# Performance work log

Hardware: AMD Instinct MI355X
Metric: run time of the kernel (lower is better)

## Reference

```python
import jax, jax.numpy as jnp
import numpy as np

V, E, H, ENC2, L_LAYERS = 1024, 512, 1024, 1024, 3
SOS, EOS = 1, 2


def lstm_cell(x, h, c, W_ih, W_hh, b_ih, b_hh):
    # PyTorch LSTMCell: gates ordered i, f, g, o
    gates = x @ W_ih.T + b_ih + h @ W_hh.T + b_hh
    i, f, g, o = jnp.split(gates, 4, axis=-1)
    i = jax.nn.sigmoid(i)
    f = jax.nn.sigmoid(f)
    g = jnp.tanh(g)
    o = jax.nn.sigmoid(o)
    c = f * c + i * g
    h = o * jnp.tanh(c)
    return h, c


def setup_inputs() -> dict:
    key = jax.random.key(0)
    ks = jax.random.split(key, 20)
    s = 0.05
    inp = {
        'tokens': jax.random.randint(ks[0], (16, 256), 0, V),
        'encoder_outputs': jax.random.normal(ks[1], (16, 512, ENC2), jnp.float32),
        'embedding': jax.random.normal(ks[2], (V, E), jnp.float32) * s,
        # layer 0: input = embedding + encoder context
        'W_ih0': jax.random.normal(ks[3], (4 * H, E + ENC2), jnp.float32) * s,
        'W_hh0': jax.random.normal(ks[4], (4 * H, H), jnp.float32) * s,
        'b_ih0': jnp.zeros((4 * H,), jnp.float32),
        'b_hh0': jnp.zeros((4 * H,), jnp.float32),
        'W_ih1': jax.random.normal(ks[5], (4 * H, H), jnp.float32) * s,
        'W_hh1': jax.random.normal(ks[6], (4 * H, H), jnp.float32) * s,
        'b_ih1': jnp.zeros((4 * H,), jnp.float32),
        'b_hh1': jnp.zeros((4 * H,), jnp.float32),
        'W_ih2': jax.random.normal(ks[7], (4 * H, H), jnp.float32) * s,
        'W_hh2': jax.random.normal(ks[8], (4 * H, H), jnp.float32) * s,
        'b_ih2': jnp.zeros((4 * H,), jnp.float32),
        'b_hh2': jnp.zeros((4 * H,), jnp.float32),
        'W1': jax.random.normal(ks[9], (H, ENC2 + H), jnp.float32) * s,
        'b1': jnp.zeros((H,), jnp.float32),
        'W2': jax.random.normal(ks[10], (V, H), jnp.float32) * s,
        'b2': jnp.zeros((V,), jnp.float32),
    }
    return inp


def reference(tokens, encoder_outputs, embedding,
              W_ih0, W_hh0, b_ih0, b_hh0,
              W_ih1, W_hh1, b_ih1, b_hh1,
              W_ih2, W_hh2, b_ih2, b_hh2,
              W1, b1, W2, b2):
    B, L = tokens.shape
    dtype = encoder_outputs.dtype
    # teacher forcing sequences: dec_in = [sos, y], dec_out = [y, eos]
    dec_in = jnp.concatenate([jnp.full((B, 1), SOS, tokens.dtype), tokens], axis=1)   # [B, T]
    dec_out = jnp.concatenate([tokens, jnp.full((B, 1), EOS, tokens.dtype)], axis=1)  # [B, T]
    T = L + 1

    emb = embedding[dec_in]  # [B, T, E]
    # NOTE: the original forward feeds initial_context (zeros) as the LSTM input
    # context at EVERY step (it is never updated), so the recurrence does not
    # depend on attention and can be scanned independently.
    xs = jnp.concatenate([emb, jnp.zeros((B, T, ENC2), dtype)], axis=-1)  # [B, T, E+ENC2]
    xs = jnp.swapaxes(xs, 0, 1)  # time-major [T, B, E+ENC2]

    z = jnp.zeros((B, H), dtype)
    init = (z, z, z, z, z, z)

    def step(carry, x_t):
        h0, c0, h1, c1, h2, c2 = carry
        h0, c0 = lstm_cell(x_t, h0, c0, W_ih0, W_hh0, b_ih0, b_hh0)
        h1, c1 = lstm_cell(h0, h1, c1, W_ih1, W_hh1, b_ih1, b_hh1)
        h2, c2 = lstm_cell(h1, h2, c2, W_ih2, W_hh2, b_ih2, b_hh2)
        return (h0, c0, h1, c1, h2, c2), h2

    _, hs = jax.lax.scan(step, init, xs)      # [T, B, H]
    hs = jnp.swapaxes(hs, 0, 1)               # [B, T, H]

    # dot-product attention over encoder outputs (vectorized over all steps)
    scores = jnp.einsum('bth,bsh->bts', hs, encoder_outputs)   # [B, T, S]
    attn = jax.nn.softmax(scores, axis=-1)
    ctx = jnp.einsum('bts,bsh->bth', attn, encoder_outputs)    # [B, T, ENC2]

    mlp_in = jnp.concatenate([hs, ctx], axis=-1)               # [B, T, H+ENC2]
    hidden = jnp.tanh(mlp_in @ W1.T + b1)
    logits = hidden @ W2.T + b2                                # [B, T, V]

    logp = jax.nn.log_softmax(logits, axis=-1)
    nll = -jnp.take_along_axis(logp, dec_out[..., None], axis=-1)[..., 0]
    return jnp.mean(nll)
```

## Files before the change

### kernel.cpp

```cpp
#include <hip/hip_runtime.h>
#include <math.h>


namespace {
constexpr int TT = 257;
constexpr int BT = 4112;
constexpr int NSTEP = 259;
constexpr int NWG = 256;

constexpr size_t OFF_EMBB = 0;
constexpr size_t OFF_H0H  = 524288;
constexpr size_t OFF_H1H  = 4751360;
constexpr size_t OFF_H2H  = 8978432;
constexpr size_t OFF_ENCB = 0;
constexpr size_t OFF_ENCT = 13205504;
constexpr size_t OFF_W1B  = 21594112;
constexpr size_t OFF_W2B  = 23691264;
constexpr size_t OFF_SC   = 24739840;
constexpr size_t OFF_CTX  = 26845184;
constexpr size_t OFF_HID  = 31055872;
constexpr size_t OFF_LG   = OFF_SC;
constexpr size_t END_BF   = 35266560;
constexpr size_t OFF_INT_BYTES = END_BF * 2;
constexpr int    ARRIVE_I0     = 12352;
constexpr int    GO_I0         = ARRIVE_I0 + 256 * 32;
constexpr size_t TOTAL_BYTES   = OFF_INT_BYTES + (GO_I0 + 16) * 4;
constexpr unsigned SPIN_CAP    = 1u << 22;
}

typedef __attribute__((ext_vector_type(8))) short bf16x8;
typedef __attribute__((ext_vector_type(4))) float f32x4;

__device__ __forceinline__ float bf2f(ushort u) {
    union { unsigned int v; float f; } x; x.v = ((unsigned int)u) << 16; return x.f;
}
__device__ __forceinline__ ushort f2bf(float f) {
    union { float f; unsigned int v; } x; x.f = f;
    return (ushort)((x.v + 0x7fff + ((x.v >> 16) & 1)) >> 16);
}
__device__ __forceinline__ float sigm(float x) { return 1.f / (1.f + __expf(-x)); }

__global__ void k_fail(float* out) { out[0] = -123456.0f; }

__global__ __launch_bounds__(256) void k_init(const int* __restrict__ tokens,
                                              const float* __restrict__ emb,
                                              ushort* __restrict__ wsb,
                                              float* __restrict__ out)
{
    int i = blockIdx.x * 256 + threadIdx.x;
    int* dec_in  = (int*)((char*)wsb + OFF_INT_BYTES);
    int* dec_out = dec_in + 4112;
    int* hsrow   = dec_in + 8224;
    unsigned* flags = (unsigned*)(dec_in + ARRIVE_I0);
    {
        size_t e = (size_t)i * 8;
        float4 a = *(const float4*)(emb + e);
        float4 b = *(const float4*)(emb + e + 4);
        uint4 o;
        o.x = (unsigned)f2bf(a.x) | ((unsigned)f2bf(a.y) << 16);
        o.y = (unsigned)f2bf(a.z) | ((unsigned)f2bf(a.w) << 16);
        o.z = (unsigned)f2bf(b.x) | ((unsigned)f2bf(b.y) << 16);
        o.w = (unsigned)f2bf(b.z) | ((unsigned)f2bf(b.w) << 16);
        *(uint4*)(wsb + OFF_EMBB + e) = o;
    }
    if (i < 16384) {
        wsb[OFF_H0H + i] = 0; wsb[OFF_H1H + i] = 0; wsb[OFF_H2H + i] = 0;
    }
    if (i < 4112) {
        int t = i >> 4, b = i & 15;
        dec_in[i] = (t == 0) ? 1 : tokens[b * 256 + (t - 1)];
        int bb = i / 257, tt = i % 257;
        dec_out[i] = (tt < 256) ? tokens[bb * 256 + tt] : 2;
        hsrow[i] = (tt + 1) * 16 + bb;
    }
    if (i < 256 * 32 + 16) flags[i] = 0u;
    if (i == 0) out[0] = 0.f;
}

__global__ __launch_bounds__(1024, 4) void k_rec_persist(
    ushort* __restrict__ wsb,
    const float* __restrict__ Whh0, const float* __restrict__ Wih0,
    const float* __restrict__ Wih1, const float* __restrict__ Whh1,
    const float* __restrict__ Wih2, const float* __restrict__ Whh2,
    const float* __restrict__ bih0, const float* __restrict__ bhh0,
    const float* __restrict__ bih1, const float* __restrict__ bhh1,
    const float* __restrict__ bih2, const float* __restrict__ bhh2,
    const int* __restrict__ dec_in,
    unsigned* __restrict__ arrive, unsigned* __restrict__ go)
{
    __shared__ float p[16][16][17];

    int tid = threadIdx.x;
    int u = blockIdx.x;
    int w = tid >> 6, lane = tid & 63, l15 = lane & 15, quad = lane >> 4;

    int cell, g0, gcnt;
    if (w < 4)       { cell = 0; g0 = w * 12; gcnt = 12; }
    else if (w < 10) { int wi = w - 4;  cell = 1;
                       g0 = (wi < 4) ? wi * 11 : 44 + (wi - 4) * 10;
                       gcnt = (wi < 4) ? 11 : 10; }
    else             { int wi = w - 10; cell = 2;
                       g0 = (wi < 4) ? wi * 11 : 44 + (wi - 4) * 10;
                       gcnt = (wi < 4) ? 11 : 10; }

    int gt = l15 >> 2, s4 = l15 & 3;
    size_t wrow = (size_t)(gt * 1024 + u * 4 + s4);

    bf16x8 wreg[12];
    #pragma unroll
    for (int gi = 0; gi < 12; ++gi) {
        if (gi < gcnt) {
            int g = g0 + gi;
            const float* src;
            if (cell == 0)
                src = (g < 32) ? Whh0 + wrow * 1024 + (size_t)g * 32
                               : Wih0 + wrow * 1536 + (size_t)(g - 32) * 32;
            else if (cell == 1)
                src = (g < 32) ? Wih1 + wrow * 1024 + (size_t)g * 32
                               : Whh1 + wrow * 1024 + (size_t)(g - 32) * 32;
            else
                src = (g < 32) ? Wih2 + wrow * 1024 + (size_t)g * 32
                               : Whh2 + wrow * 1024 + (size_t)(g - 32) * 32;
            src += quad * 8;
            float4 a = *(const float4*)src;
            float4 b = *(const float4*)(src + 4);
            bf16x8 v;
            v[0] = (short)f2bf(a.x); v[1] = (short)f2bf(a.y);
            v[2] = (short)f2bf(a.z); v[3] = (short)f2bf(a.w);
            v[4] = (short)f2bf(b.x); v[5] = (short)f2bf(b.y);
            v[6] = (short)f2bf(b.z); v[7] = (short)f2bf(b.w);
            wreg[gi] = v;
        }
    }

    int cellE = tid >> 6;
    int sub = tid & 63, bE = sub & 15, sE = sub >> 4;
    int colE = u * 4 + sE;
    float bsum[4] = {0.f, 0.f, 0.f, 0.f};
    float cst = 0.f;
    ushort* hE = nullptr;
    int wloE = 0, whiE = 0;
    if (tid < 192) {
        const float* biE = (cellE == 0) ? bih0 : (cellE == 1) ? bih1 : bih2;
        const float* bhE = (cellE == 0) ? bhh0 : (cellE == 1) ? bhh1 : bhh2;
        #pragma unroll
        for (int gq = 0; gq < 4; ++gq)
            bsum[gq] = biE[gq * 1024 + colE] + bhE[gq * 1024 + colE];
        hE = wsb + ((cellE == 0) ? OFF_H0H : (cellE == 1) ? OFF_H1H : OFF_H2H);
        wloE = (cellE == 0) ? 0 : (cellE == 1) ? 4 : 10;
        whiE = (cellE == 0) ? 4 : (cellE == 1) ? 10 : 16;
    }

    ushort* h0h = wsb + OFF_H0H;
    ushort* h1h = wsb + OFF_H1H;
    ushort* h2h = wsb + OFF_H2H;
    const ushort* embB = wsb + OFF_EMBB;
    size_t aoff = (size_t)l15 * 1024 + quad * 8;

    int tokv = 0;
    if (cell == 0) tokv = dec_in[l15];

    for (int d = 0; d < NSTEP; ++d) {
        int t = d - cell;
        f32x4 acc = {0.f, 0.f, 0.f, 0.f};
        if (t >= 0 && t < TT) {
            const ushort* a0p;
            const ushort* a1p;
            if (cell == 0) {
                a0p = h0h + (size_t)t * 16384 + aoff;
                a1p = embB + (size_t)tokv * 512 + quad * 8;
                int tn = (t + 1 < TT) ? (t + 1) : (TT - 1);
                tokv = dec_in[tn * 16 + l15];
            } else if (cell == 1) {
                a0p = h0h + (size_t)(t + 1) * 16384 + aoff;
                a1p = h1h + (size_t)t * 16384 + aoff;
            } else {
                a0p = h1h + (size_t)(t + 1) * 16384 + aoff;
                a1p = h2h + (size_t)t * 16384 + aoff;
            }
            #pragma unroll
            for (int gi = 0; gi < 12; ++gi) {
                if (gi < gcnt) {
                    int g = g0 + gi;
                    bf16x8 af = (g < 32)
                        ? *(const bf16x8*)(a0p + (size_t)g * 32)
                        : *(const bf16x8*)(a1p + (size_t)(g - 32) * 32);
                    acc = __builtin_amdgcn_mfma_f32_16x16x32_bf16(
                        af, wreg[gi], acc, 0, 0, 0);
                }
            }
        }
        #pragma unroll
        for (int r = 0; r < 4; ++r) p[w][quad * 4 + r][l15] = acc[r];
        __syncthreads();

        if (tid < 192) {
            int tE = d - cellE;
            if (tE >= 0 && tE < TT) {
                float gv[4];
                #pragma unroll
                for (int gq = 0; gq < 4; ++gq) {
                    float a2 = bsum[gq];
                    for (int ww = wloE; ww < whiE; ++ww)
                        a2 += p[ww][bE][gq * 4 + sE];
                    gv[gq] = a2;
                }
                float ig = sigm(gv[0]), fg = sigm(gv[1]);
                float gg = tanhf(gv[2]), og = sigm(gv[3]);
                cst = fg * cst + ig * gg;
                ushort hus = f2bf(og * tanhf(cst));
                unsigned hi = __shfl_down((unsigned)hus, 16, 64);
                if ((sE & 1) == 0) {
                    unsigned* hp = (unsigned*)(hE + (size_t)(tE + 1) * 16384
                                               + (size_t)bE * 1024 + colE);
                    __hip_atomic_store(hp, (unsigned)hus | (hi << 16),
                                       __ATOMIC_RELAXED, __HIP_MEMORY_SCOPE_AGENT);
                }
            }
        }

        asm volatile("s_waitcnt vmcnt(0)" ::: "memory");
        __syncthreads();
        unsigned stamp = (unsigned)(d + 1);
        if (u == 0) {
            if (tid > 0 && tid < 256) {
                unsigned spins = 0;
                while (__hip_atomic_load(arrive + tid * 32, __ATOMIC_RELAXED,
                                         __HIP_MEMORY_SCOPE_AGENT) < stamp) {
                    if (++spins > SPIN_CAP) break;
                }
            }
            __syncthreads();
            if (tid == 0)
                __hip_atomic_store(go, stamp, __ATOMIC_RELAXED,
                                   __HIP_MEMORY_SCOPE_AGENT);
        } else {
            if (tid == 0) {
                __hip_atomic_store(arrive + u * 32, stamp, __ATOMIC_RELAXED,
                                   __HIP_MEMORY_SCOPE_AGENT);
                unsigned spins = 0;
                while (__hip_atomic_load(go, __ATOMIC_RELAXED,
                                         __HIP_MEMORY_SCOPE_AGENT) < stamp) {
                    __builtin_amdgcn_s_sleep(1);
                    if (++spins > SPIN_CAP) break;
                }
            }
            __syncthreads();
        }
    }
}

__global__ __launch_bounds__(256) void k_cvt_flat(const float* __restrict__ src,
                                                  ushort* __restrict__ dst)
{
    size_t e = ((size_t)blockIdx.x * 256 + threadIdx.x) * 8;
    float4 a = *(const float4*)(src + e);
    float4 b = *(const float4*)(src + e + 4);
    uint4 o;
    o.x = (unsigned)f2bf(a.x) | ((unsigned)f2bf(a.y) << 16);
    o.y = (unsigned)f2bf(a.z) | ((unsigned)f2bf(a.w) << 16);
    o.z = (unsigned)f2bf(b.x) | ((unsigned)f2bf(b.y) << 16);
    o.w = (unsigned)f2bf(b.z) | ((unsigned)f2bf(b.w) << 16);
    *(uint4*)(dst + e) = o;
}

__global__ __launch_bounds__(256) void k_enc_t(const float* __restrict__ enc,
                                               ushort* __restrict__ encT)
{
    __shared__ float tile[32][33];
    int b = blockIdx.z, s0 = blockIdx.x * 32, h0 = blockIdx.y * 32;
    int tx = threadIdx.x & 31, ty = threadIdx.x >> 5;
    const float* src = enc + (size_t)b * 524288;
    #pragma unroll
    for (int i = 0; i < 4; i++) {
        int s = s0 + ty + i * 8;
        tile[ty + i * 8][tx] = src[(size_t)s * 1024 + h0 + tx];
    }
    __syncthreads();
    ushort* dst = encT + (size_t)b * 524288;
    #pragma unroll
    for (int i = 0; i < 4; i++) {
        int h = h0 + ty + i * 8;
        dst[(size_t)h * 512 + s0 + tx] = f2bf(tile[tx][ty + i * 8]);
    }
}

__global__ __launch_bounds__(256) void k_gemm_bb(
    const ushort* __restrict__ A, int lda, long sA, const int* __restrict__ aIdx,
    const ushort* __restrict__ B, int ldb, long sB,
    ushort* __restrict__ C, int ldc, long sC,
    int M, int K, int accum)
{
    int z = blockIdx.z;
    const ushort* Ab = A + (size_t)z * sA;
    const ushort* Bb = B + (size_t)z * sB;
    ushort* Cb = C + (size_t)z * sC;
    int m0 = blockIdx.y * 64, n0 = blockIdx.x * 64;
    int tid = threadIdx.x, w = tid >> 6, lane = tid & 63;
    int l15 = lane & 15, quad = lane >> 4;
    int am = m0 + w * 16 + l15;
    int ar = (am < M) ? (aIdx ? aIdx[am] : am) : (aIdx ? aIdx[0] : 0);
    const ushort* ap = Ab + (size_t)ar * lda + quad * 8;
    const ushort* bp = Bb + (size_t)(n0 + l15) * ldb + quad * 8;
    f32x4 acc[4] = {{0.f,0.f,0.f,0.f},{0.f,0.f,0.f,0.f},{0.f,0.f,0.f,0.f},{0.f,0.f,0.f,0.f}};
    for (int k0 = 0; k0 < K; k0 += 32) {
        bf16x8 af = *(const bf16x8*)(ap + k0);
        #pragma unroll
        for (int j = 0; j < 4; j++) {
            bf16x8 bfb = *(const bf16x8*)(bp + (size_t)j * 16 * ldb + k0);
            acc[j] = __builtin_amdgcn_mfma_f32_16x16x32_bf16(af, bfb, acc[j], 0, 0, 0);
        }
    }
    #pragma unroll
    for (int j = 0; j < 4; j++)
        #pragma unroll
        for (int r = 0; r < 4; r++) {
            int row = m0 + w * 16 + quad * 4 + r;
            if (row < M) {
                ushort* cp = Cb + (size_t)row * ldc + n0 + j * 16 + l15;
                float v = acc[j][r];
                if (accum) v += bf2f(*cp);
                *cp = f2bf(v);
            }
        }
}

__global__ __launch_bounds__(256) void k_softmax_b(ushort* __restrict__ sc)
{
    __shared__ float red[4];
    ushort* p = sc + (size_t)blockIdx.x * 512;
    int tid = threadIdx.x;
    float a = bf2f(p[tid]), b = bf2f(p[tid + 256]);
    float m = fmaxf(a, b);
    for (int o = 32; o; o >>= 1) m = fmaxf(m, __shfl_xor(m, o, 64));
    if ((tid & 63) == 0) red[tid >> 6] = m;
    __syncthreads();
    m = fmaxf(fmaxf(red[0], red[1]), fmaxf(red[2], red[3]));
    __syncthreads();
    float ea = __expf(a - m), eb = __expf(b - m);
    float s = ea + eb;
    for (int o = 32; o; o >>= 1) s += __shfl_xor(s, o, 64);
    if ((tid & 63) == 0) red[tid >> 6] = s;
    __syncthreads();
    s = red[0] + red[1] + red[2] + red[3];
    float inv = 1.f / s;
    p[tid] = f2bf(ea * inv);
    p[tid + 256] = f2bf(eb * inv);
}

__global__ __launch_bounds__(256) void k_tanh_bias_b(ushort* __restrict__ hid,
                                                     const float* __restrict__ b1)
{
    size_t i = (size_t)blockIdx.x * 256 + threadIdx.x;
    hid[i] = f2bf(tanhf(bf2f(hid[i]) + b1[i & 1023]));
}

__global__ __launch_bounds__(256) void k_loss_b(const ushort* __restrict__ logits,
                                                const float* __restrict__ b2,
                                                const int* __restrict__ dec_out_m,
                                                float* __restrict__ out)
{
    __shared__ float red[4];
    int m = blockIdx.x;
    const ushort* p = logits + (size_t)m * 1024;
    int tid = threadIdx.x;
    float v0 = bf2f(p[tid]) + b2[tid];
    float v1 = bf2f(p[tid + 256]) + b2[tid + 256];
    float v2 = bf2f(p[tid + 512]) + b2[tid + 512];
    float v3 = bf2f(p[tid + 768]) + b2[tid + 768];
    float mx = fmaxf(fmaxf(v0, v1), fmaxf(v2, v3));
    for (int o = 32; o; o >>= 1) mx = fmaxf(mx, __shfl_xor(mx, o, 64));
    if ((tid & 63) == 0) red[tid >> 6] = mx;
    __syncthreads();
    mx = fmaxf(fmaxf(red[0], red[1]), fmaxf(red[2], red[3]));
    __syncthreads();
    float s = __expf(v0 - mx) + __expf(v1 - mx) + __expf(v2 - mx) + __expf(v3 - mx);
    for (int o = 32; o; o >>= 1) s += __shfl_xor(s, o, 64);
    if ((tid & 63) == 0) red[tid >> 6] = s;
    __syncthreads();
    if (tid == 0) {
        float ssum = red[0] + red[1] + red[2] + red[3];
        int tgt = dec_out_m[m];
        float tv = bf2f(p[tgt]) + b2[tgt];
        atomicAdd(out, (mx + logf(ssum) - tv) * (1.0f / 4112.0f));
    }
}

extern "C" void kernel_launch(void* const* d_in, const int* in_sizes, int n_in,
                              void* d_out, int out_size, void* d_ws, size_t ws_size,
                              hipStream_t stream)
{
    const int*   tokens = (const int*)d_in[0];
    const float* enc    = (const float*)d_in[1];
    const float* emb    = (const float*)d_in[2];
    const float* Wih0   = (const float*)d_in[3];
    const float* Whh0   = (const float*)d_in[4];
    const float* bih0   = (const float*)d_in[5];
    const float* bhh0   = (const float*)d_in[6];
    const float* Wih1   = (const float*)d_in[7];
    const float* Whh1   = (const float*)d_in[8];
    const float* bih1   = (const float*)d_in[9];
    const float* bhh1   = (const float*)d_in[10];
    const float* Wih2   = (const float*)d_in[11];
    const float* Whh2   = (const float*)d_in[12];
    const float* bih2   = (const float*)d_in[13];
    const float* bhh2   = (const float*)d_in[14];
    const float* W1     = (const float*)d_in[15];
    const float* b1     = (const float*)d_in[16];
    const float* W2     = (const float*)d_in[17];
    const float* b2     = (const float*)d_in[18];

    float* out = (float*)d_out;
    if (ws_size < TOTAL_BYTES) { k_fail<<<1, 1, 0, stream>>>(out); return; }

    ushort* wsb  = (ushort*)d_ws;
    ushort* h2h  = wsb + OFF_H2H;
    ushort* sc   = wsb + OFF_SC;
    ushort* ctx  = wsb + OFF_CTX;
    ushort* hid  = wsb + OFF_HID;
    ushort* lg   = wsb + OFF_LG;
    ushort* encB = wsb + OFF_ENCB;
    ushort* encT = wsb + OFF_ENCT;
    ushort* W1b  = wsb + OFF_W1B;
    ushort* W2b  = wsb + OFF_W2B;
    int* dec_in  = (int*)((char*)d_ws + OFF_INT_BYTES);
    int* dec_out = dec_in + 4112;
    int* hsrow   = dec_in + 8224;
    unsigned* arrive = (unsigned*)(dec_in + ARRIVE_I0);
    unsigned* go     = (unsigned*)(dec_in + GO_I0);

    k_init<<<256, 256, 0, stream>>>(tokens, emb, wsb, out);

    k_rec_persist<<<NWG, 1024, 0, stream>>>(wsb, Whh0, Wih0, Wih1, Whh1,
                                            Wih2, Whh2, bih0, bhh0, bih1, bhh1,
                                            bih2, bhh2, dec_in, arrive, go);

    k_cvt_flat<<<4096, 256, 0, stream>>>(enc, encB);
    k_enc_t<<<dim3(16, 32, 16), 256, 0, stream>>>(enc, encT);
    k_cvt_flat<<<1024, 256, 0, stream>>>(W1, W1b);
    k_cvt_flat<<<512, 256, 0, stream>>>(W2, W2b);

    k_gemm_bb<<<dim3(8, 5, 16), 256, 0, stream>>>(h2h + 16384, 16384, 1024, nullptr,
                                                  encB, 1024, 524288,
                                                  sc, 512, 131584, TT, 1024, 0);
    k_softmax_b<<<4112, 256, 0, stream>>>(sc);
    k_gemm_bb<<<dim3(16, 5, 16), 256, 0, stream>>>(sc, 512, 131584, nullptr,
                                                   encT, 512, 524288,
                                                   ctx, 1024, 263168, TT, 512, 0);
    k_gemm_bb<<<dim3(16, 65, 1), 256, 0, stream>>>(h2h, 1024, 0, hsrow,
                                                   W1b, 2048, 0,
                                                   hid, 1024, 0, BT, 1024, 0);
    k_gemm_bb<<<dim3(16, 65, 1), 256, 0, stream>>>(ctx, 1024, 0, nullptr,
                                                   W1b + 1024, 2048, 0,
                                                   hid, 1024, 0, BT, 1024, 1);
    k_tanh_bias_b<<<16448, 256, 0, stream>>>(hid, b1);
    k_gemm_bb<<<dim3(16, 65, 1), 256, 0, stream>>>(hid, 1024, 0, nullptr,
                                                   W2b, 1024, 0,
                                                   lg, 1024, 0, BT, 1024, 0);
    k_loss_b<<<4112, 256, 0, stream>>>(lg, b2, dec_out, out);
}
```

Before: 3.083 ms.

## Fuse W1 two-part GEMM with bias and tanh; widen recurrent h stores

Replaces the two accumulating W1 GEMMs and the separate tanh+bias pass with one dual-input GEMM kernel that applies bias and tanh in its epilogue. This removes a bf16 round trip of the hidden buffer and two kernel launches. Separately, the recurrent kernel now packs four bf16 hidden values into one 64-bit atomic store instead of two per 32-bit store, halving the store count. The dual kernel has no LDS tiling, so global load efficiency is the same as the old GEMM.

Result: no change. 3.132 ms (+1.6%).

```diff
diff --git a/kernel.cpp b/kernel.cpp
--- a/kernel.cpp
+++ b/kernel.cpp
@@ -209,12 +209,16 @@
                 float gg = tanhf(gv[2]), og = sigm(gv[3]);
                 cst = fg * cst + ig * gg;
                 ushort hus = f2bf(og * tanhf(cst));
-                unsigned hi = __shfl_down((unsigned)hus, 16, 64);
-                if ((sE & 1) == 0) {
-                    unsigned* hp = (unsigned*)(hE + (size_t)(tE + 1) * 16384
-                                               + (size_t)bE * 1024 + colE);
-                    __hip_atomic_store(hp, (unsigned)hus | (hi << 16),
-                                       __ATOMIC_RELAXED, __HIP_MEMORY_SCOPE_AGENT);
+                unsigned pair  = (unsigned)hus
+                               | (__shfl_down((unsigned)hus, 16, 64) << 16);
+                unsigned pair2 = __shfl_down(pair, 32, 64);
+                if (sE == 0) {
+                    unsigned long long v = (unsigned long long)pair
+                                         | ((unsigned long long)pair2 << 32);
+                    unsigned long long* hp = (unsigned long long*)
+                        (hE + (size_t)(tE + 1) * 16384 + (size_t)bE * 1024 + colE);
+                    __hip_atomic_store(hp, v, __ATOMIC_RELAXED,
+                                       __HIP_MEMORY_SCOPE_AGENT);
                 }
             }
         }
@@ -325,6 +329,49 @@
         }
 }
 
+__global__ __launch_bounds__(256) void k_gemm_dual(
+    const ushort* __restrict__ A1, const int* __restrict__ aIdx,
+    const ushort* __restrict__ A2,
+    const ushort* __restrict__ B1, const ushort* __restrict__ B2,
+    const float* __restrict__ bias, ushort* __restrict__ C, int M)
+{
+    int m0 = blockIdx.y * 64, n0 = blockIdx.x * 64;
+    int tid = threadIdx.x, w = tid >> 6, lane = tid & 63;
+    int l15 = lane & 15, quad = lane >> 4;
+    int am = m0 + w * 16 + l15;
+    int ar  = (am < M) ? aIdx[am] : aIdx[0];
+    int am2 = (am < M) ? am : 0;
+    const ushort* ap1 = A1 + (size_t)ar  * 1024 + quad * 8;
+    const ushort* ap2 = A2 + (size_t)am2 * 1024 + quad * 8;
+    const ushort* bp1 = B1 + (size_t)(n0 + l15) * 2048 + quad * 8;
+    const ushort* bp2 = B2 + (size_t)(n0 + l15) * 2048 + quad * 8;
+    f32x4 acc[4] = {{0.f,0.f,0.f,0.f},{0.f,0.f,0.f,0.f},{0.f,0.f,0.f,0.f},{0.f,0.f,0.f,0.f}};
+    for (int k0 = 0; k0 < 1024; k0 += 32) {
+        bf16x8 a1 = *(const bf16x8*)(ap1 + k0);
+        bf16x8 a2 = *(const bf16x8*)(ap2 + k0);
+        #pragma unroll
+        for (int j = 0; j < 4; j++) {
+            bf16x8 b1f = *(const bf16x8*)(bp1 + (size_t)j * 16 * 2048 + k0);
+            acc[j] = __builtin_amdgcn_mfma_f32_16x16x32_bf16(a1, b1f, acc[j], 0, 0, 0);
+        }
+        #pragma unroll
+        for (int j = 0; j < 4; j++) {
+            bf16x8 b2f = *(const bf16x8*)(bp2 + (size_t)j * 16 * 2048 + k0);
+            acc[j] = __builtin_amdgcn_mfma_f32_16x16x32_bf16(a2, b2f, acc[j], 0, 0, 0);
+        }
+    }
+    #pragma unroll
+    for (int j = 0; j < 4; j++)
+        #pragma unroll
+        for (int r = 0; r < 4; r++) {
+            int row = m0 + w * 16 + quad * 4 + r;
+            if (row < M) {
+                int col = n0 + j * 16 + l15;
+                C[(size_t)row * 1024 + col] = f2bf(tanhf(acc[j][r] + bias[col]));
+            }
+        }
+}
+
 __global__ __launch_bounds__(256) void k_softmax_b(ushort* __restrict__ sc)
 {
     __shared__ float red[4];
@@ -346,13 +393,6 @@
     float inv = 1.f / s;
     p[tid] = f2bf(ea * inv);
     p[tid + 256] = f2bf(eb * inv);
-}
-
-__global__ __launch_bounds__(256) void k_tanh_bias_b(ushort* __restrict__ hid,
-                                                     const float* __restrict__ b1)
-{
-    size_t i = (size_t)blockIdx.x * 256 + threadIdx.x;
-    hid[i] = f2bf(tanhf(bf2f(hid[i]) + b1[i & 1023]));
 }
 
 __global__ __launch_bounds__(256) void k_loss_b(const ushort* __restrict__ logits,
@@ -447,13 +487,9 @@
     k_gemm_bb<<<dim3(16, 5, 16), 256, 0, stream>>>(sc, 512, 131584, nullptr,
                                                    encT, 512, 524288,
                                                    ctx, 1024, 263168, TT, 512, 0);
-    k_gemm_bb<<<dim3(16, 65, 1), 256, 0, stream>>>(h2h, 1024, 0, hsrow,
-                                                   W1b, 2048, 0,
-                                                   hid, 1024, 0, BT, 1024, 0);
-    k_gemm_bb<<<dim3(16, 65, 1), 256, 0, stream>>>(ctx, 1024, 0, nullptr,
-                                                   W1b + 1024, 2048, 0,
-                                                   hid, 1024, 0, BT, 1024, 1);
-    k_tanh_bias_b<<<16448, 256, 0, stream>>>(hid, b1);
+    k_gemm_dual<<<dim3(16, 65, 1), 256, 0, stream>>>(h2h, hsrow, ctx,
+                                                     W1b, W1b + 1024, b1,
+                                                     hid, BT);
     k_gemm_bb<<<dim3(16, 65, 1), 256, 0, stream>>>(hid, 1024, 0, nullptr,
                                                    W2b, 1024, 0,
                                                    lg, 1024, 0, BT, 1024, 0);
```
